# Kernel tuning notes

Measured on AMD Instinct MI355X. Metric: run time of the kernel, lower is better.

Reference implementation:

```python
import jax, jax.numpy as jnp
import numpy as np

B, J, D = 64, 512, 1024

def setup_inputs() -> dict:
    key = jax.random.key(0)
    k_x, k_m, k1, k2, k3 = jax.random.split(key, 5)
    x = jax.random.normal(k_x, (B, J, D), dtype=jnp.float32)
    mask = (jax.random.uniform(k_m, (B, J)) > 0.1).astype(jnp.float32)
    s1 = 1.0 / np.sqrt(D)
    W1 = jax.random.uniform(k1, (D, D), minval=-s1, maxval=s1, dtype=jnp.float32)
    b1 = jnp.zeros((D,), jnp.float32)
    W2 = jax.random.uniform(k2, (D, 1), minval=-s1, maxval=s1, dtype=jnp.float32)
    b2 = jnp.zeros((1,), jnp.float32)
    W3 = jax.random.uniform(k3, (D, 3), minval=-s1, maxval=s1, dtype=jnp.float32)
    b3 = jnp.zeros((3,), jnp.float32)
    return {"x": x, "mask": mask, "W1": W1, "b1": b1, "W2": W2, "b2": b2, "W3": W3, "b3": b3}

def reference(x, mask, W1, b1, W2, b2, W3, b3):
    # MLP attention scoring: linear1 -> tanh -> linear2 -> sigmoid
    h = jnp.tanh(jnp.einsum('bjd,de->bje', x, W1) + b1)          # [B,J,D]
    val = jax.nn.sigmoid(jnp.einsum('bjd,do->bjo', h, W2) + b2)  # [B,J,1]
    val = val * mask[:, :, None]                                  # mask out pads
    inv_sum = 1.0 / jnp.sum(val, axis=(1, 2))                     # [B]
    att_weights = val * inv_sum[:, None, None]                    # [B,J,1]
    pooled = jnp.einsum('bjk,bjm->bk', x, att_weights)            # [B,D]
    output_val = pooled @ W3 + b3                                 # [B,3]
    return output_val, att_weights
```

## Files before the change

### kernel.cpp

```cpp
#include <hip/hip_runtime.h>
#include <math.h>
#include <stdint.h>

#define B_ 64
#define J_ 512
#define D_ 1024

typedef __attribute__((ext_vector_type(8))) short short8;
typedef __attribute__((ext_vector_type(4))) float f32x4;

#define GLOBAL_AS __attribute__((address_space(1)))
#define LDS_AS    __attribute__((address_space(3)))

__device__ __forceinline__ void async16(const void* g, void* l) {
    __builtin_amdgcn_global_load_lds((const GLOBAL_AS uint32_t*)g,
                                     (LDS_AS uint32_t*)l, 16, 0, 0);
}

__device__ __forceinline__ float fast_tanh(float x) {
    return 1.0f - 2.0f / (1.0f + __expf(2.0f * x));
}

__device__ __forceinline__ unsigned short f2bf(float f) {
    uint32_t u = __builtin_bit_cast(uint32_t, f);
    u += 0x7fffu + ((u >> 16) & 1u);
    return (unsigned short)(u >> 16);
}

__device__ __forceinline__ uint32_t pk2(float a, float b) {
    return (uint32_t)f2bf(a) | ((uint32_t)f2bf(b) << 16);
}

__global__ __launch_bounds__(256) void transpose_cast_w1(const float* __restrict__ W1,
                                                         unsigned short* __restrict__ W1t) {
    __shared__ float t[32][33];
    const int n = blockIdx.x * 32 + threadIdx.x;
    for (int i = threadIdx.y; i < 32; i += 8)
        t[i][threadIdx.x] = W1[(size_t)(blockIdx.y * 32 + i) * D_ + n];
    __syncthreads();
    const int k = blockIdx.y * 32 + threadIdx.x;
    for (int i = threadIdx.y; i < 32; i += 8)
        W1t[(size_t)(blockIdx.x * 32 + i) * D_ + k] = f2bf(t[threadIdx.x][i]);
}

__global__ __launch_bounds__(512, 4) void gemm_score_kernel(
    const float* __restrict__ x, const unsigned short* __restrict__ W1t,
    const float* __restrict__ b1, const float* __restrict__ W2,
    const float* __restrict__ b2, const float* __restrict__ mask,
    float* __restrict__ val_ws, float* __restrict__ pooled)
{
    __shared__ __align__(16) unsigned short ldsA[64 * 64];
    __shared__ __align__(16) unsigned short ldsB[2 * 256 * 64];
    __shared__ float pv_part[8][64];
    __shared__ float vrow[64];

    const int tid  = threadIdx.x;
    const int wave = tid >> 6;
    const int l    = tid & 63;
    const int wn   = wave;
    const int l15  = l & 15;
    const int kgrp = l >> 4;
    const int l7   = l & 7;
    const int r0   = blockIdx.x * 64;
    const int bb   = r0 >> 9;

    const int arow = tid >> 3;
    const int achv = ((tid & 7) ^ (arow & 7)) << 3;
    const float* gAf = x + (size_t)(r0 + arow) * D_ + achv;
    unsigned short* lA = ldsA + tid * 8;

    const unsigned short* gB[4];
    unsigned short* lB[4];
    #pragma unroll
    for (int t = 0; t < 4; ++t) {
        const int f = tid + t * 512;
        const int row = f >> 3;
        const int ch = ((f & 7) ^ (row & 7)) << 3;
        gB[t] = W1t + (size_t)row * D_ + ch;
        lB[t] = ldsB + t * 4096 + (wave << 9);
    }

    int aoff[4][2], boff[2][2];
    #pragma unroll
    for (int mi = 0; mi < 4; ++mi)
        #pragma unroll
        for (int ks = 0; ks < 2; ++ks)
            aoff[mi][ks] = (mi * 16 + l15) * 64 + (((ks * 4 + kgrp) ^ l7) << 3);
    #pragma unroll
    for (int ni = 0; ni < 2; ++ni)
        #pragma unroll
        for (int ks = 0; ks < 2; ++ks)
            boff[ni][ks] = (wn * 32 + ni * 16 + l15) * 64 + (((ks * 4 + kgrp) ^ l7) << 3);

    float pv[4][4];
    #pragma unroll
    for (int mi = 0; mi < 4; ++mi)
        #pragma unroll
        for (int r = 0; r < 4; ++r) pv[mi][r] = 0.f;

    f32x4 acc[4][2];
    #pragma unroll
    for (int mi = 0; mi < 4; ++mi)
        #pragma unroll
        for (int ni = 0; ni < 2; ++ni)
            acc[mi][ni] = (f32x4){0.f, 0.f, 0.f, 0.f};

    float4 fA0 = *reinterpret_cast<const float4*>(gAf);
    float4 fA1 = *reinterpret_cast<const float4*>(gAf + 4);
    #pragma unroll
    for (int t = 0; t < 4; ++t) async16(gB[t], lB[t]);
    uint32_t apk0 = pk2(fA0.x, fA0.y);
    uint32_t apk1 = pk2(fA0.z, fA0.w);
    uint32_t apk2 = pk2(fA1.x, fA1.y);
    uint32_t apk3 = pk2(fA1.z, fA1.w);

    for (int it = 0; it < 64; ++it) {
        const int cur = it & 1;

        __syncthreads();

        *reinterpret_cast<uint4*>(lA) = (uint4){apk0, apk1, apk2, apk3};

        if (it < 63) {
            const int nit  = it + 1;
            const int nk0  = (nit & 15) << 6;
            const size_t nbofs = (size_t)(nit >> 4) * 256 * D_ + nk0;
            fA0 = *reinterpret_cast<const float4*>(gAf + nk0);
            fA1 = *reinterpret_cast<const float4*>(gAf + nk0 + 4);
            const int nbuf = (cur ^ 1) << 14;
            #pragma unroll
            for (int t = 0; t < 4; ++t) async16(gB[t] + nbofs, lB[t] + nbuf);
        }

        asm volatile("s_waitcnt lgkmcnt(0)" ::: "memory");
        __builtin_amdgcn_s_barrier();
        asm volatile("" ::: "memory");

        const int bo = cur << 14;
        #pragma unroll
        for (int ks = 0; ks < 2; ++ks) {
            const short8 a0 = *reinterpret_cast<const short8*>(ldsA + aoff[0][ks]);
            const short8 a1 = *reinterpret_cast<const short8*>(ldsA + aoff[1][ks]);
            const short8 a2 = *reinterpret_cast<const short8*>(ldsA + aoff[2][ks]);
            const short8 a3 = *reinterpret_cast<const short8*>(ldsA + aoff[3][ks]);
            const short8 b0 = *reinterpret_cast<const short8*>(ldsB + bo + boff[0][ks]);
            const short8 b1f = *reinterpret_cast<const short8*>(ldsB + bo + boff[1][ks]);
            acc[0][0] = __builtin_amdgcn_mfma_f32_16x16x32_bf16(a0, b0,  acc[0][0], 0, 0, 0);
            acc[1][0] = __builtin_amdgcn_mfma_f32_16x16x32_bf16(a1, b0,  acc[1][0], 0, 0, 0);
            acc[2][0] = __builtin_amdgcn_mfma_f32_16x16x32_bf16(a2, b0,  acc[2][0], 0, 0, 0);
            acc[3][0] = __builtin_amdgcn_mfma_f32_16x16x32_bf16(a3, b0,  acc[3][0], 0, 0, 0);
            acc[0][1] = __builtin_amdgcn_mfma_f32_16x16x32_bf16(a0, b1f, acc[0][1], 0, 0, 0);
            acc[1][1] = __builtin_amdgcn_mfma_f32_16x16x32_bf16(a1, b1f, acc[1][1], 0, 0, 0);
            acc[2][1] = __builtin_amdgcn_mfma_f32_16x16x32_bf16(a2, b1f, acc[2][1], 0, 0, 0);
            acc[3][1] = __builtin_amdgcn_mfma_f32_16x16x32_bf16(a3, b1f, acc[3][1], 0, 0, 0);
        }

        if (it < 63) {
            apk0 = pk2(fA0.x, fA0.y);
            apk1 = pk2(fA0.z, fA0.w);
            apk2 = pk2(fA1.x, fA1.y);
            apk3 = pk2(fA1.z, fA1.w);
        }

        if ((it & 15) == 15) {
            const int n0 = it >> 4;
            #pragma unroll
            for (int ni = 0; ni < 2; ++ni) {
                const int col = n0 * 256 + wn * 32 + ni * 16 + l15;
                const float b1v = b1[col];
                const float w2v = W2[col];
                #pragma unroll
                for (int mi = 0; mi < 4; ++mi)
                    #pragma unroll
                    for (int r = 0; r < 4; ++r) {
                        const float h = fast_tanh(acc[mi][ni][r] + b1v);
                        pv[mi][r] = fmaf(h, w2v, pv[mi][r]);
                        acc[mi][ni][r] = 0.f;
                    }
            }
        }
    }

    #pragma unroll
    for (int mi = 0; mi < 4; ++mi)
        #pragma unroll
        for (int r = 0; r < 4; ++r) {
            float s = pv[mi][r];
            s += __shfl_xor(s, 1);
            s += __shfl_xor(s, 2);
            s += __shfl_xor(s, 4);
            s += __shfl_xor(s, 8);
            if (l15 == 0) pv_part[wn][mi * 16 + kgrp * 4 + r] = s;
        }
    __syncthreads();
    if (tid < 64) {
        float s = b2[0];
        #pragma unroll
        for (int w = 0; w < 8; ++w) s += pv_part[w][tid];
        const float sg = 1.0f / (1.0f + __expf(-s));
        const float v = sg * mask[r0 + tid];
        val_ws[r0 + tid] = v;
        vrow[tid] = v;
    }
    __syncthreads();

    const int kc = tid << 1;
    float a0 = 0.f, a1 = 0.f;
    for (int row = 0; row < 64; ++row) {
        const float v = vrow[row];
        const float2 xv = *reinterpret_cast<const float2*>(
            x + (size_t)(r0 + row) * D_ + kc);
        a0 = fmaf(xv.x, v, a0);
        a1 = fmaf(xv.y, v, a1);
    }
    atomicAdd(&pooled[bb * D_ + kc], a0);
    atomicAdd(&pooled[bb * D_ + kc + 1], a1);
}

#define MT 64
#define KT 32
#define PAD 68

__global__ __launch_bounds__(256) void score_kernel_fp32(
    const float* __restrict__ x, const float* __restrict__ mask,
    const float* __restrict__ W1, const float* __restrict__ b1,
    const float* __restrict__ W2, const float* __restrict__ b2,
    float* __restrict__ val_ws, float* __restrict__ pooled)
{
    __shared__ float As[KT][PAD];
    __shared__ float Bs[KT][PAD];
    __shared__ float red[MT][17];
    __shared__ float vrow[MT];

    const int tid = threadIdx.x;
    const int tx = tid & 15;
    const int ty = tid >> 4;
    const int r0 = blockIdx.x * MT;
    const int b  = r0 >> 9;

    float pv[4] = {0.f, 0.f, 0.f, 0.f};

    for (int n0 = 0; n0 < D_; n0 += 64) {
        float acc[4][4];
        #pragma unroll
        for (int i = 0; i < 4; ++i)
            #pragma unroll
            for (int j = 0; j < 4; ++j) acc[i][j] = 0.f;

        for (int k0 = 0; k0 < D_; k0 += KT) {
            #pragma unroll
            for (int ll = 0; ll < 2; ++ll) {
                const int f   = tid + ll * 256;
                const int row = f >> 3;
                const int k4  = (f & 7) << 2;
                const float4 xv = *reinterpret_cast<const float4*>(
                    &x[(size_t)(r0 + row) * D_ + k0 + k4]);
                As[k4 + 0][row] = xv.x;
                As[k4 + 1][row] = xv.y;
                As[k4 + 2][row] = xv.z;
                As[k4 + 3][row] = xv.w;
            }
            #pragma unroll
            for (int ll = 0; ll < 2; ++ll) {
                const int f  = tid + ll * 256;
                const int k  = f >> 4;
                const int n4 = (f & 15) << 2;
                const float4 wv = *reinterpret_cast<const float4*>(
                    &W1[(size_t)(k0 + k) * D_ + n0 + n4]);
                *reinterpret_cast<float4*>(&Bs[k][n4]) = wv;
            }
            __syncthreads();
            #pragma unroll
            for (int kk = 0; kk < KT; ++kk) {
                const float4 a4 = *reinterpret_cast<const float4*>(&As[kk][ty << 2]);
                const float4 b4 = *reinterpret_cast<const float4*>(&Bs[kk][tx << 2]);
                const float av[4] = {a4.x, a4.y, a4.z, a4.w};
                const float bv[4] = {b4.x, b4.y, b4.z, b4.w};
                #pragma unroll
                for (int i = 0; i < 4; ++i)
                    #pragma unroll
                    for (int j = 0; j < 4; ++j)
                        acc[i][j] = fmaf(av[i], bv[j], acc[i][j]);
            }
            __syncthreads();
        }
        #pragma unroll
        for (int j = 0; j < 4; ++j) {
            const int col = n0 + (tx << 2) + j;
            const float b1v = b1[col];
            const float w2v = W2[col];
            #pragma unroll
            for (int i = 0; i < 4; ++i) {
                const float h = fast_tanh(acc[i][j] + b1v);
                pv[i] = fmaf(h, w2v, pv[i]);
            }
        }
    }

    #pragma unroll
    for (int i = 0; i < 4; ++i) red[(ty << 2) + i][tx] = pv[i];
    __syncthreads();

    if (tid < MT) {
        float s = 0.f;
        #pragma unroll
        for (int t = 0; t < 16; ++t) s += red[tid][t];
        const float z  = s + b2[0];
        const float sg = 1.0f / (1.0f + __expf(-z));
        const float v  = sg * mask[r0 + tid];
        val_ws[r0 + tid] = v;
        vrow[tid] = v;
    }
    __syncthreads();

    const int k = tid << 2;
    float a0 = 0.f, a1 = 0.f, a2 = 0.f, a3 = 0.f;
    for (int row = 0; row < MT; ++row) {
        const float v = vrow[row];
        const float4 xv = *reinterpret_cast<const float4*>(
            &x[(size_t)(r0 + row) * D_ + k]);
        a0 = fmaf(xv.x, v, a0);
        a1 = fmaf(xv.y, v, a1);
        a2 = fmaf(xv.z, v, a2);
        a3 = fmaf(xv.w, v, a3);
    }
    float* pb = &pooled[b * D_ + k];
    atomicAdd(pb + 0, a0);
    atomicAdd(pb + 1, a1);
    atomicAdd(pb + 2, a2);
    atomicAdd(pb + 3, a3);
}

__global__ __launch_bounds__(256) void finalize_kernel(
    const float* __restrict__ val_ws, const float* __restrict__ pooled,
    const float* __restrict__ W3, const float* __restrict__ b3,
    float* __restrict__ out)
{
    __shared__ float sred[256];
    const int b = blockIdx.x;
    const int tid = threadIdx.x;

    const float v0 = val_ws[b * J_ + tid];
    const float v1 = val_ws[b * J_ + 256 + tid];
    sred[tid] = v0 + v1;
    __syncthreads();
    for (int s = 128; s > 0; s >>= 1) {
        if (tid < s) sred[tid] += sred[tid + s];
        __syncthreads();
    }
    const float inv = 1.0f / sred[0];

    out[192 + b * J_ + tid]       = v0 * inv;
    out[192 + b * J_ + 256 + tid] = v1 * inv;

    const int k = tid << 2;
    float acc3[3] = {0.f, 0.f, 0.f};
    #pragma unroll
    for (int c = 0; c < 4; ++c) {
        const float p = pooled[b * D_ + k + c] * inv;
        acc3[0] = fmaf(p, W3[(k + c) * 3 + 0], acc3[0]);
        acc3[1] = fmaf(p, W3[(k + c) * 3 + 1], acc3[1]);
        acc3[2] = fmaf(p, W3[(k + c) * 3 + 2], acc3[2]);
    }
    for (int o = 0; o < 3; ++o) {
        __syncthreads();
        sred[tid] = acc3[o];
        __syncthreads();
        for (int s = 128; s > 0; s >>= 1) {
            if (tid < s) sred[tid] += sred[tid + s];
            __syncthreads();
        }
        if (tid == 0) out[b * 3 + o] = sred[0] + b3[o];
    }
}

extern "C" void kernel_launch(void* const* d_in, const int* in_sizes, int n_in,
                              void* d_out, int out_size, void* d_ws, size_t ws_size,
                              hipStream_t stream) {
    const float* x    = (const float*)d_in[0];
    const float* mask = (const float*)d_in[1];
    const float* W1   = (const float*)d_in[2];
    const float* b1   = (const float*)d_in[3];
    const float* W2   = (const float*)d_in[4];
    const float* b2   = (const float*)d_in[5];
    const float* W3   = (const float*)d_in[6];
    const float* b3   = (const float*)d_in[7];
    float* out = (float*)d_out;

    const size_t W1T_BYTES  = (size_t)D_ * D_ * 2;
    const size_t VAL_BYTES  = (size_t)B_ * J_ * 4;
    const size_t POOL_BYTES = (size_t)B_ * D_ * 4;
    const size_t NEED = W1T_BYTES + VAL_BYTES + POOL_BYTES;

    if (ws_size >= NEED) {
        unsigned short* W1t = (unsigned short*)d_ws;
        float* val_ws = (float*)((char*)d_ws + W1T_BYTES);
        float* pooled = (float*)((char*)d_ws + W1T_BYTES + VAL_BYTES);

        hipMemsetAsync(pooled, 0, POOL_BYTES, stream);
        transpose_cast_w1<<<dim3(32, 32), dim3(32, 8), 0, stream>>>(W1, W1t);
        gemm_score_kernel<<<512, 512, 0, stream>>>(x, W1t, b1, W2, b2, mask,
                                                   val_ws, pooled);
        finalize_kernel<<<B_, 256, 0, stream>>>(val_ws, pooled, W3, b3, out);
    } else {
        float* val_ws = (float*)d_ws;
        float* pooled = val_ws + B_ * J_;
        hipMemsetAsync(pooled, 0, POOL_BYTES, stream);
        score_kernel_fp32<<<(B_ * J_) / MT, 256, 0, stream>>>(
            x, mask, W1, b1, W2, b2, val_ws, pooled);
        finalize_kernel<<<B_, 256, 0, stream>>>(val_ws, pooled, W3, b3, out);
    }
}
```

Baseline: 315.9 us.

## Cache bf16 x in workspace, widen per-wave N tile, fuse memset into prep

The GEMM kernel now uses 256 threads with each wave covering 64 output columns (a 4x4 MFMA tile) instead of 32. On the first N-pass it converts x to bf16 and writes it to a workspace buffer, and later passes and the pooling stage read that half-size copy instead of re-reading and re-converting fp32 x. The pooled memset is folded into the W1 transpose/cast kernel, and s_setprio is raised around the MFMA block. Together these cut global traffic and conversion work and remove one launch. In exchange the kernel needs a 64 MB extra workspace and has higher register pressure. Pooling now uses bf16-rounded x, which slightly changes numerics.

```diff
diff --git a/kernel.cpp b/kernel.cpp
--- a/kernel.cpp
+++ b/kernel.cpp
@@ -31,66 +31,78 @@
     return (uint32_t)f2bf(a) | ((uint32_t)f2bf(b) << 16);
 }
 
-__global__ __launch_bounds__(256) void transpose_cast_w1(const float* __restrict__ W1,
-                                                         unsigned short* __restrict__ W1t) {
+__global__ __launch_bounds__(256) void prep_kernel(const float* __restrict__ W1,
+                                                   unsigned short* __restrict__ W1t,
+                                                   float* __restrict__ pooled) {
     __shared__ float t[32][33];
-    const int n = blockIdx.x * 32 + threadIdx.x;
-    for (int i = threadIdx.y; i < 32; i += 8)
-        t[i][threadIdx.x] = W1[(size_t)(blockIdx.y * 32 + i) * D_ + n];
-    __syncthreads();
-    const int k = blockIdx.y * 32 + threadIdx.x;
-    for (int i = threadIdx.y; i < 32; i += 8)
-        W1t[(size_t)(blockIdx.x * 32 + i) * D_ + k] = f2bf(t[threadIdx.x][i]);
-}
-
-__global__ __launch_bounds__(512, 4) void gemm_score_kernel(
-    const float* __restrict__ x, const unsigned short* __restrict__ W1t,
+    const int b   = blockIdx.x;
+    const int tid = threadIdx.x;
+    if (b < 256) pooled[b * 256 + tid] = 0.f;
+    const int bx = b & 31, by = b >> 5;
+    const int tx = tid & 31, ty = tid >> 5;
+    const int n = bx * 32 + tx;
+    for (int i = ty; i < 32; i += 8)
+        t[i][tx] = W1[(size_t)(by * 32 + i) * D_ + n];
+    __syncthreads();
+    const int k = by * 32 + tx;
+    for (int i = ty; i < 32; i += 8)
+        W1t[(size_t)(bx * 32 + i) * D_ + k] = f2bf(t[tx][i]);
+}
+
+__global__ __launch_bounds__(256, 2) void gemm_score_kernel(
+    const float* __restrict__ x, unsigned short* __restrict__ Xb,
+    const unsigned short* __restrict__ W1t,
     const float* __restrict__ b1, const float* __restrict__ W2,
     const float* __restrict__ b2, const float* __restrict__ mask,
     float* __restrict__ val_ws, float* __restrict__ pooled)
 {
     __shared__ __align__(16) unsigned short ldsA[64 * 64];
     __shared__ __align__(16) unsigned short ldsB[2 * 256 * 64];
-    __shared__ float pv_part[8][64];
-    __shared__ float vrow[64];
 
     const int tid  = threadIdx.x;
     const int wave = tid >> 6;
     const int l    = tid & 63;
-    const int wn   = wave;
     const int l15  = l & 15;
     const int kgrp = l >> 4;
     const int l7   = l & 7;
     const int r0   = blockIdx.x * 64;
     const int bb   = r0 >> 9;
 
-    const int arow = tid >> 3;
-    const int achv = ((tid & 7) ^ (arow & 7)) << 3;
-    const float* gAf = x + (size_t)(r0 + arow) * D_ + achv;
-    unsigned short* lA = ldsA + tid * 8;
-
-    const unsigned short* gB[4];
-    unsigned short* lB[4];
-    #pragma unroll
-    for (int t = 0; t < 4; ++t) {
-        const int f = tid + t * 512;
+    const float* gAx[2];
+    unsigned short* gXb[2];
+    int lAoff[2];
+    #pragma unroll
+    for (int t = 0; t < 2; ++t) {
+        const int f   = tid + t * 256;
         const int row = f >> 3;
-        const int ch = ((f & 7) ^ (row & 7)) << 3;
+        const int ch  = ((f & 7) ^ (row & 7)) << 3;
+        gAx[t]   = x  + (size_t)(r0 + row) * D_ + ch;
+        gXb[t]   = Xb + (size_t)(r0 + row) * D_ + ch;
+        lAoff[t] = f * 8;
+    }
+
+    const unsigned short* gB[8];
+    unsigned short* lB[8];
+    #pragma unroll
+    for (int t = 0; t < 8; ++t) {
+        const int f   = tid + t * 256;
+        const int row = f >> 3;
+        const int ch  = ((f & 7) ^ (row & 7)) << 3;
         gB[t] = W1t + (size_t)row * D_ + ch;
-        lB[t] = ldsB + t * 4096 + (wave << 9);
-    }
-
-    int aoff[4][2], boff[2][2];
+        lB[t] = ldsB + t * 2048 + (wave << 9);
+    }
+
+    int aoff[4][2], boff[4][2];
     #pragma unroll
     for (int mi = 0; mi < 4; ++mi)
         #pragma unroll
         for (int ks = 0; ks < 2; ++ks)
             aoff[mi][ks] = (mi * 16 + l15) * 64 + (((ks * 4 + kgrp) ^ l7) << 3);
     #pragma unroll
-    for (int ni = 0; ni < 2; ++ni)
+    for (int ni = 0; ni < 4; ++ni)
         #pragma unroll
         for (int ks = 0; ks < 2; ++ks)
-            boff[ni][ks] = (wn * 32 + ni * 16 + l15) * 64 + (((ks * 4 + kgrp) ^ l7) << 3);
+            boff[ni][ks] = (wave * 64 + ni * 16 + l15) * 64 + (((ks * 4 + kgrp) ^ l7) << 3);
 
     float pv[4][4];
     #pragma unroll
@@ -98,38 +110,57 @@
         #pragma unroll
         for (int r = 0; r < 4; ++r) pv[mi][r] = 0.f;
 
-    f32x4 acc[4][2];
+    f32x4 acc[4][4];
     #pragma unroll
     for (int mi = 0; mi < 4; ++mi)
         #pragma unroll
-        for (int ni = 0; ni < 2; ++ni)
+        for (int ni = 0; ni < 4; ++ni)
             acc[mi][ni] = (f32x4){0.f, 0.f, 0.f, 0.f};
 
-    float4 fA0 = *reinterpret_cast<const float4*>(gAf);
-    float4 fA1 = *reinterpret_cast<const float4*>(gAf + 4);
-    #pragma unroll
-    for (int t = 0; t < 4; ++t) async16(gB[t], lB[t]);
-    uint32_t apk0 = pk2(fA0.x, fA0.y);
-    uint32_t apk1 = pk2(fA0.z, fA0.w);
-    uint32_t apk2 = pk2(fA1.x, fA1.y);
-    uint32_t apk3 = pk2(fA1.z, fA1.w);
+    uint4 curA0, curA1;
+    {
+        const float4 p0 = *reinterpret_cast<const float4*>(gAx[0]);
+        const float4 p1 = *reinterpret_cast<const float4*>(gAx[0] + 4);
+        const float4 p2 = *reinterpret_cast<const float4*>(gAx[1]);
+        const float4 p3 = *reinterpret_cast<const float4*>(gAx[1] + 4);
+        curA0 = (uint4){pk2(p0.x, p0.y), pk2(p0.z, p0.w), pk2(p1.x, p1.y), pk2(p1.z, p1.w)};
+        curA1 = (uint4){pk2(p2.x, p2.y), pk2(p2.z, p2.w), pk2(p3.x, p3.y), pk2(p3.z, p3.w)};
+    }
+    #pragma unroll
+    for (int t = 0; t < 8; ++t) async16(gB[t], lB[t]);
+
+    float4 fa0, fa1, fa2, fa3;
+    uint4 nxA0, nxA1;
 
     for (int it = 0; it < 64; ++it) {
         const int cur = it & 1;
 
         __syncthreads();
 
-        *reinterpret_cast<uint4*>(lA) = (uint4){apk0, apk1, apk2, apk3};
-
-        if (it < 63) {
-            const int nit  = it + 1;
-            const int nk0  = (nit & 15) << 6;
-            const size_t nbofs = (size_t)(nit >> 4) * 256 * D_ + nk0;
-            fA0 = *reinterpret_cast<const float4*>(gAf + nk0);
-            fA1 = *reinterpret_cast<const float4*>(gAf + nk0 + 4);
-            const int nbuf = (cur ^ 1) << 14;
-            #pragma unroll
-            for (int t = 0; t < 4; ++t) async16(gB[t] + nbofs, lB[t] + nbuf);
+        *reinterpret_cast<uint4*>(ldsA + lAoff[0]) = curA0;
+        *reinterpret_cast<uint4*>(ldsA + lAoff[1]) = curA1;
+        if (it < 16) {
+            const int k0 = it << 6;
+            *reinterpret_cast<uint4*>(gXb[0] + k0) = curA0;
+            *reinterpret_cast<uint4*>(gXb[1] + k0) = curA1;
+        }
+
+        const int nit = it + 1;
+        if (nit < 64) {
+            const int ak0 = (nit & 15) << 6;
+            if (nit < 16) {
+                fa0 = *reinterpret_cast<const float4*>(gAx[0] + ak0);
+                fa1 = *reinterpret_cast<const float4*>(gAx[0] + ak0 + 4);
+                fa2 = *reinterpret_cast<const float4*>(gAx[1] + ak0);
+                fa3 = *reinterpret_cast<const float4*>(gAx[1] + ak0 + 4);
+            } else {
+                nxA0 = *reinterpret_cast<const uint4*>(gXb[0] + ak0);
+                nxA1 = *reinterpret_cast<const uint4*>(gXb[1] + ak0);
+            }
+            const size_t bofs = (size_t)(nit >> 4) * 256 * D_ + ak0;
+            const int nb = (cur ^ 1) << 14;
+            #pragma unroll
+            for (int t = 0; t < 8; ++t) async16(gB[t] + bofs, lB[t] + nb);
         }
 
         asm volatile("s_waitcnt lgkmcnt(0)" ::: "memory");
@@ -137,14 +168,17 @@
         asm volatile("" ::: "memory");
 
         const int bo = cur << 14;
+        __builtin_amdgcn_s_setprio(1);
         #pragma unroll
         for (int ks = 0; ks < 2; ++ks) {
-            const short8 a0 = *reinterpret_cast<const short8*>(ldsA + aoff[0][ks]);
-            const short8 a1 = *reinterpret_cast<const short8*>(ldsA + aoff[1][ks]);
-            const short8 a2 = *reinterpret_cast<const short8*>(ldsA + aoff[2][ks]);
-            const short8 a3 = *reinterpret_cast<const short8*>(ldsA + aoff[3][ks]);
-            const short8 b0 = *reinterpret_cast<const short8*>(ldsB + bo + boff[0][ks]);
-            const short8 b1f = *reinterpret_cast<const short8*>(ldsB + bo + boff[1][ks]);
+            short8 a0 = *reinterpret_cast<const short8*>(ldsA + aoff[0][ks]);
+            short8 a1 = *reinterpret_cast<const short8*>(ldsA + aoff[1][ks]);
+            short8 a2 = *reinterpret_cast<const short8*>(ldsA + aoff[2][ks]);
+            short8 a3 = *reinterpret_cast<const short8*>(ldsA + aoff[3][ks]);
+            short8 b0 = *reinterpret_cast<const short8*>(ldsB + bo + boff[0][ks]);
+            short8 b1f = *reinterpret_cast<const short8*>(ldsB + bo + boff[1][ks]);
+            short8 b2f = *reinterpret_cast<const short8*>(ldsB + bo + boff[2][ks]);
+            short8 b3f = *reinterpret_cast<const short8*>(ldsB + bo + boff[3][ks]);
             acc[0][0] = __builtin_amdgcn_mfma_f32_16x16x32_bf16(a0, b0,  acc[0][0], 0, 0, 0);
             acc[1][0] = __builtin_amdgcn_mfma_f32_16x16x32_bf16(a1, b0,  acc[1][0], 0, 0, 0);
             acc[2][0] = __builtin_amdgcn_mfma_f32_16x16x32_bf16(a2, b0,  acc[2][0], 0, 0, 0);
@@ -153,20 +187,34 @@
             acc[1][1] = __builtin_amdgcn_mfma_f32_16x16x32_bf16(a1, b1f, acc[1][1], 0, 0, 0);
             acc[2][1] = __builtin_amdgcn_mfma_f32_16x16x32_bf16(a2, b1f, acc[2][1], 0, 0, 0);
             acc[3][1] = __builtin_amdgcn_mfma_f32_16x16x32_bf16(a3, b1f, acc[3][1], 0, 0, 0);
-        }
-
-        if (it < 63) {
-            apk0 = pk2(fA0.x, fA0.y);
-            apk1 = pk2(fA0.z, fA0.w);
-            apk2 = pk2(fA1.x, fA1.y);
-            apk3 = pk2(fA1.z, fA1.w);
+            acc[0][2] = __builtin_amdgcn_mfma_f32_16x16x32_bf16(a0, b2f, acc[0][2], 0, 0, 0);
+            acc[1][2] = __builtin_amdgcn_mfma_f32_16x16x32_bf16(a1, b2f, acc[1][2], 0, 0, 0);
+            acc[2][2] = __builtin_amdgcn_mfma_f32_16x16x32_bf16(a2, b2f, acc[2][2], 0, 0, 0);
+            acc[3][2] = __builtin_amdgcn_mfma_f32_16x16x32_bf16(a3, b2f, acc[3][2], 0, 0, 0);
+            acc[0][3] = __builtin_amdgcn_mfma_f32_16x16x32_bf16(a0, b3f, acc[0][3], 0, 0, 0);
+            acc[1][3] = __builtin_amdgcn_mfma_f32_16x16x32_bf16(a1, b3f, acc[1][3], 0, 0, 0);
+            acc[2][3] = __builtin_amdgcn_mfma_f32_16x16x32_bf16(a2, b3f, acc[2][3], 0, 0, 0);
+            acc[3][3] = __builtin_amdgcn_mfma_f32_16x16x32_bf16(a3, b3f, acc[3][3], 0, 0, 0);
+        }
+        __builtin_amdgcn_s_setprio(0);
+
+        if (nit < 64) {
+            if (nit < 16) {
+                curA0 = (uint4){pk2(fa0.x, fa0.y), pk2(fa0.z, fa0.w),
+                                pk2(fa1.x, fa1.y), pk2(fa1.z, fa1.w)};
+                curA1 = (uint4){pk2(fa2.x, fa2.y), pk2(fa2.z, fa2.w),
+                                pk2(fa3.x, fa3.y), pk2(fa3.z, fa3.w)};
+            } else {
+                curA0 = nxA0;
+                curA1 = nxA1;
+            }
         }
 
         if ((it & 15) == 15) {
             const int n0 = it >> 4;
             #pragma unroll
-            for (int ni = 0; ni < 2; ++ni) {
-                const int col = n0 * 256 + wn * 32 + ni * 16 + l15;
+            for (int ni = 0; ni < 4; ++ni) {
+                const int col = n0 * 256 + wave * 64 + ni * 16 + l15;
                 const float b1v = b1[col];
                 const float w2v = W2[col];
                 #pragma unroll
@@ -181,6 +229,10 @@
         }
     }
 
+    __syncthreads();
+    float* pv_part = reinterpret_cast<float*>(ldsA);
+    float* vrow    = pv_part + 256;
+
     #pragma unroll
     for (int mi = 0; mi < 4; ++mi)
         #pragma unroll
@@ -190,13 +242,12 @@
             s += __shfl_xor(s, 2);
             s += __shfl_xor(s, 4);
             s += __shfl_xor(s, 8);
-            if (l15 == 0) pv_part[wn][mi * 16 + kgrp * 4 + r] = s;
+            if (l15 == 0) pv_part[wave * 64 + mi * 16 + kgrp * 4 + r] = s;
         }
     __syncthreads();
     if (tid < 64) {
-        float s = b2[0];
-        #pragma unroll
-        for (int w = 0; w < 8; ++w) s += pv_part[w][tid];
+        const float s = b2[0] + pv_part[tid] + pv_part[64 + tid]
+                      + pv_part[128 + tid] + pv_part[192 + tid];
         const float sg = 1.0f / (1.0f + __expf(-s));
         const float v = sg * mask[r0 + tid];
         val_ws[r0 + tid] = v;
@@ -204,17 +255,22 @@
     }
     __syncthreads();
 
-    const int kc = tid << 1;
-    float a0 = 0.f, a1 = 0.f;
+    const int kc = tid << 2;
+    float a0 = 0.f, a1 = 0.f, a2 = 0.f, a3 = 0.f;
     for (int row = 0; row < 64; ++row) {
         const float v = vrow[row];
-        const float2 xv = *reinterpret_cast<const float2*>(
-            x + (size_t)(r0 + row) * D_ + kc);
-        a0 = fmaf(xv.x, v, a0);
-        a1 = fmaf(xv.y, v, a1);
-    }
-    atomicAdd(&pooled[bb * D_ + kc], a0);
-    atomicAdd(&pooled[bb * D_ + kc + 1], a1);
+        const uint2 u = *reinterpret_cast<const uint2*>(
+            Xb + (size_t)(r0 + row) * D_ + kc);
+        a0 = fmaf(__builtin_bit_cast(float, u.x << 16), v, a0);
+        a1 = fmaf(__builtin_bit_cast(float, u.x & 0xffff0000u), v, a1);
+        a2 = fmaf(__builtin_bit_cast(float, u.y << 16), v, a2);
+        a3 = fmaf(__builtin_bit_cast(float, u.y & 0xffff0000u), v, a3);
+    }
+    float* pb = &pooled[bb * D_ + kc];
+    atomicAdd(pb + 0, a0);
+    atomicAdd(pb + 1, a1);
+    atomicAdd(pb + 2, a2);
+    atomicAdd(pb + 3, a3);
 }
 
 #define MT 64
@@ -387,19 +443,20 @@
     const float* b3   = (const float*)d_in[7];
     float* out = (float*)d_out;
 
+    const size_t XB_BYTES   = (size_t)B_ * J_ * D_ * 2;
     const size_t W1T_BYTES  = (size_t)D_ * D_ * 2;
     const size_t VAL_BYTES  = (size_t)B_ * J_ * 4;
     const size_t POOL_BYTES = (size_t)B_ * D_ * 4;
-    const size_t NEED = W1T_BYTES + VAL_BYTES + POOL_BYTES;
+    const size_t NEED = XB_BYTES + W1T_BYTES + VAL_BYTES + POOL_BYTES;
 
     if (ws_size >= NEED) {
-        unsigned short* W1t = (unsigned short*)d_ws;
-        float* val_ws = (float*)((char*)d_ws + W1T_BYTES);
-        float* pooled = (float*)((char*)d_ws + W1T_BYTES + VAL_BYTES);
-
-        hipMemsetAsync(pooled, 0, POOL_BYTES, stream);
-        transpose_cast_w1<<<dim3(32, 32), dim3(32, 8), 0, stream>>>(W1, W1t);
-        gemm_score_kernel<<<512, 512, 0, stream>>>(x, W1t, b1, W2, b2, mask,
+        unsigned short* Xb  = (unsigned short*)d_ws;
+        unsigned short* W1t = (unsigned short*)((char*)d_ws + XB_BYTES);
+        float* val_ws = (float*)((char*)d_ws + XB_BYTES + W1T_BYTES);
+        float* pooled = (float*)((char*)d_ws + XB_BYTES + W1T_BYTES + VAL_BYTES);
+
+        prep_kernel<<<1024, 256, 0, stream>>>(W1, W1t, pooled);
+        gemm_score_kernel<<<512, 256, 0, stream>>>(x, Xb, W1t, b1, W2, b2, mask,
                                                    val_ws, pooled);
         finalize_kernel<<<B_, 256, 0, stream>>>(val_ws, pooled, W3, b3, out);
     } else {
```

Measured after the change: 327.5 us. +3.6%, slower.
